# Optimization experiments

Hardware: AMD Instinct MI355X
Metric: run time of the kernel (lower is better)

Reference implementation:

```python
import jax, jax.numpy as jnp
import numpy as np

B, TM1, D, H = 1024, 255, 128, 128  # batch, n_timestep-1, input_size, hidden_size


def setup_inputs() -> dict:
    key = jax.random.key(0)
    ks = jax.random.split(key, 7)
    s = 0.05
    return {
        "input_data": jax.random.normal(ks[0], (B, TM1, D), jnp.float32),
        "Wa": jax.random.normal(ks[1], (1, 2 * H + TM1), jnp.float32) * s,
        "ba": jax.random.normal(ks[2], (1,), jnp.float32) * s,
        "W_ih": jax.random.normal(ks[3], (4 * H, D), jnp.float32) * s,
        "W_hh": jax.random.normal(ks[4], (4 * H, H), jnp.float32) * s,
        "b_ih": jax.random.normal(ks[5], (4 * H,), jnp.float32) * s,
        "b_hh": jax.random.normal(ks[6], (4 * H,), jnp.float32) * s,
    }


def _encoder(input_data, Wa, ba, W_ih, W_hh, b_ih, b_hh):
    b, tm1, d = input_data.shape
    h_dim = W_hh.shape[1]
    # Split attention weight into hidden / cell / time-series parts.
    Wh, Wc, Wx = Wa[0, :h_dim], Wa[0, h_dim:2 * h_dim], Wa[0, 2 * h_dim:]
    # Contribution of the (constant across steps) full driving series: (B, D)
    x_part = jnp.einsum("btd,t->bd", input_data, Wx)

    def step(carry, x_t):  # x_t: (B, D) = input_data[:, t, :]
        h, c = carry  # each (B, H)
        # attn score[b, d] = Wh.h[b] + Wc.c[b] + Wx.x[b, :, d] + ba  -> (B, D)
        score = x_part + (h @ Wh)[:, None] + (c @ Wc)[:, None] + ba[0]
        attn = jax.nn.softmax(score, axis=1)
        wx = attn * x_t  # weighted input (B, D)
        # single LSTM cell step, PyTorch gate order i, f, g, o
        gates = wx @ W_ih.T + b_ih + h @ W_hh.T + b_hh  # (B, 4H)
        i, f, g, o = jnp.split(gates, 4, axis=1)
        c_new = jax.nn.sigmoid(f) * c + jax.nn.sigmoid(i) * jnp.tanh(g)
        h_new = jax.nn.sigmoid(o) * jnp.tanh(c_new)
        return (h_new, c_new), (wx, h_new)

    h0 = jnp.zeros((b, h_dim), input_data.dtype)
    c0 = jnp.zeros((b, h_dim), input_data.dtype)
    xs = jnp.transpose(input_data, (1, 0, 2))  # (T-1, B, D)
    _, (wts, enc) = jax.lax.scan(step, (h0, c0), xs)
    input_weighted = jnp.transpose(wts, (1, 0, 2))  # (B, T-1, D)
    input_encoded = jnp.transpose(enc, (1, 0, 2))   # (B, T-1, H)
    return input_weighted, input_encoded


def reference(input_data, Wa, ba, W_ih, W_hh, b_ih, b_hh):
    return _encoder(input_data, Wa, ba, W_ih, W_hh, b_ih, b_hh)
```

## Files before the change

kernel.cpp:

```cpp
#include <hip/hip_runtime.h>
#include <hip/hip_bf16.h>
#include <stdint.h>

#define B_ 1024
#define T_ 255
#define D_ 128

typedef float f32x4 __attribute__((ext_vector_type(4)));
typedef short s16x8 __attribute__((ext_vector_type(8)));
typedef unsigned u32x4 __attribute__((ext_vector_type(4)));

__device__ __forceinline__ unsigned pk2(float a, float b){
  __hip_bfloat162 h2 = __float22bfloat162_rn(make_float2(a, b));
  union { __hip_bfloat162 h; unsigned u; } c; c.h = h2; return c.u;
}
__device__ __forceinline__ unsigned short bf1(float a){
  __hip_bfloat16 h = __float2bfloat16(a);
  union { __hip_bfloat16 h; unsigned short u; } c; c.h = h; return c.u;
}
__device__ __forceinline__ float sigm_f(float x){
  return __builtin_amdgcn_rcpf(1.f + __expf(-x));
}
__device__ __forceinline__ float tanh_f2(float x){
  return fmaf(-2.f, __builtin_amdgcn_rcpf(1.f + __expf(2.f * x)), 1.f);
}

__global__ __launch_bounds__(512) void k_attn(const float* __restrict__ x,
    const float* __restrict__ Wa, float* __restrict__ out_w,
    uint2* __restrict__ wxq){
  extern __shared__ float4 xs4[];
  __shared__ float wxs[256];
  __shared__ float part_s[16][128];
  __shared__ float red[128];
  __shared__ float attn_s[128];
  int tid = threadIdx.x, b = blockIdx.x;
  if (tid < T_) wxs[tid] = Wa[2 * D_ + tid];
  __syncthreads();
  const float4* xg = (const float4*)(x + (size_t)b * T_ * D_);
  float4 acc = {0.f, 0.f, 0.f, 0.f};
  for (int i = tid; i < 8160; i += 512){
    float4 v = xg[i];
    xs4[i] = v;
    float wt = wxs[i >> 5];
    acc.x += v.x * wt; acc.y += v.y * wt; acc.z += v.z * wt; acc.w += v.w * wt;
  }
  int d0 = (tid & 31) * 4, s = tid >> 5;
  *(float4*)&part_s[s][d0] = acc;
  __syncthreads();
  if (tid < 128){
    float v = 0.f;
    #pragma unroll
    for (int k = 0; k < 16; k++) v += part_s[k][tid];
    red[tid] = v; attn_s[tid] = v;
  }
  __syncthreads();
  for (int st = 64; st >= 1; st >>= 1){
    if (tid < st) red[tid] = fmaxf(red[tid], red[tid + st]);
    __syncthreads();
  }
  float mx = red[0];
  __syncthreads();
  float ev = 0.f;
  if (tid < 128){ ev = __expf(attn_s[tid] - mx); red[tid] = ev; }
  __syncthreads();
  for (int st = 64; st >= 1; st >>= 1){
    if (tid < st) red[tid] += red[tid + st];
    __syncthreads();
  }
  float sm = red[0];
  if (tid < 128) attn_s[tid] = ev / sm;
  __syncthreads();
  float4 at = *(const float4*)&attn_s[d0];
  float4* owg = (float4*)(out_w + (size_t)b * T_ * D_);
  for (int i = tid; i < 8160; i += 512){
    float4 v = xs4[i];
    float4 wv; wv.x = v.x*at.x; wv.y = v.y*at.y; wv.z = v.z*at.z; wv.w = v.w*at.w;
    owg[i] = wv;
    int t = i >> 5;
    uint2 q;
    q.x = pk2(wv.x, wv.y);
    q.y = pk2(wv.z, wv.w);
    wxq[((size_t)t * B_ + b) * 32 + (i & 31)] = q;
  }
}

__global__ __launch_bounds__(512, 2) void k_rnn(const float* __restrict__ W_ih,
    const float* __restrict__ W_hh, const float* __restrict__ b_ih,
    const float* __restrict__ b_hh, const unsigned short* __restrict__ wxb,
    float* __restrict__ out_e){
  __shared__ char hl[2048];
  __shared__ float4 g1l[2048];
  int tid = threadIdx.x;
  int lane = tid & 63, w = tid >> 6;
  int l15 = lane & 15, lg = lane >> 4;
  int row0 = blockIdx.x << 2;
  int d = w * 16 + l15;
  int hr = l15 >> 2;

  s16x8 fih[4][4], fhh[4][4];
  float bias[4];
  #pragma unroll
  for (int g = 0; g < 4; g++){
    int n = g * 128 + w * 16 + l15;
    bias[g] = b_ih[n] + b_hh[n];
    #pragma unroll
    for (int kt = 0; kt < 4; kt++){
      const float4* p1 = (const float4*)(W_ih + n * D_ + kt * 32 + lg * 8);
      float4 a0 = p1[0], a1 = p1[1];
      u32x4 bv;
      bv[0] = pk2(a0.x, a0.y); bv[1] = pk2(a0.z, a0.w);
      bv[2] = pk2(a1.x, a1.y); bv[3] = pk2(a1.z, a1.w);
      fih[kt][g] = __builtin_bit_cast(s16x8, bv);
      const float4* p2 = (const float4*)(W_hh + n * D_ + kt * 32 + lg * 8);
      float4 c0v = p2[0], c1v = p2[1];
      u32x4 cv;
      cv[0] = pk2(c0v.x, c0v.y); cv[1] = pk2(c0v.z, c0v.w);
      cv[2] = pk2(c1v.x, c1v.y); cv[3] = pk2(c1v.z, c1v.w);
      fhh[kt][g] = __builtin_bit_cast(s16x8, cv);
    }
  }
  unsigned rd_[4];
  #pragma unroll
  for (int kt = 0; kt < 4; kt++)
    rd_[kt] = (unsigned)(hr * 256 + (((kt << 2) + lg) ^ ((hr & 1) << 2)) * 16);
  unsigned wr_ = (unsigned)(lg * 256 + ((d >> 3) ^ ((lg & 1) << 2)) * 16 + (d & 7) * 2);

  float* op = out_e + (size_t)(row0 + lg) * T_ * D_ + d;
  float cst = 0.f;
  if (tid < 128) ((uint2*)hl)[tid] = make_uint2(0u, 0u);

  int gw0 = lg * 512 + d;
  int gr0 = lg * 128 + d;

  const unsigned short* wpb = wxb + ((size_t)(l15 >> 2) * B_ + row0 + (l15 & 3)) * D_ + lg * 8;
  const size_t GSTRIDE = (size_t)4 * B_ * D_;
  s16x8 AF0[4], AF1[4];
  #pragma unroll
  for (int kt = 0; kt < 4; kt++) AF0[kt] = *(const s16x8*)(wpb + kt * 32);
  #pragma unroll
  for (int kt = 0; kt < 4; kt++) AF1[kt] = *(const s16x8*)(wpb + GSTRIDE + kt * 32);
  __syncthreads();

#define BAR() do {                                                                  \
    asm volatile("s_waitcnt lgkmcnt(0)" ::: "memory");                              \
    __builtin_amdgcn_s_barrier();                                                   \
  } while (0)

#define FIH_BATCH(AF) do {                                                          \
    f32x4 bi = {bias[0], bias[0], bias[0], bias[0]};                                \
    f32x4 bf = {bias[1], bias[1], bias[1], bias[1]};                                \
    f32x4 bg = {bias[2], bias[2], bias[2], bias[2]};                                \
    f32x4 bo = {bias[3], bias[3], bias[3], bias[3]};                                \
    _Pragma("unroll")                                                               \
    for (int kt = 0; kt < 4; kt++){                                                 \
      bi = __builtin_amdgcn_mfma_f32_16x16x32_bf16(AF[kt], fih[kt][0], bi,0,0,0);   \
      bf = __builtin_amdgcn_mfma_f32_16x16x32_bf16(AF[kt], fih[kt][1], bf,0,0,0);   \
      bg = __builtin_amdgcn_mfma_f32_16x16x32_bf16(AF[kt], fih[kt][2], bg,0,0,0);   \
      bo = __builtin_amdgcn_mfma_f32_16x16x32_bf16(AF[kt], fih[kt][3], bo,0,0,0);   \
    }                                                                               \
    _Pragma("unroll")                                                               \
    for (int r = 0; r < 4; r++)                                                     \
      g1l[gw0 + r * 128] = make_float4(bi[r], bf[r], bg[r], bo[r]);                 \
  } while (0)

#define STEP(TS) do {                                                               \
    s16x8 aa[4];                                                                    \
    _Pragma("unroll")                                                               \
    for (int kt = 0; kt < 4; kt++)                                                  \
      aa[kt] = *(const s16x8*)(hl + rd_[kt] + ((TS) & 1) * 1024);                   \
    f32x4 a0 = {0.f,0.f,0.f,0.f}, a1 = a0, a2 = a0, a3 = a0;                        \
    _Pragma("unroll")                                                               \
    for (int kt = 0; kt < 4; kt++){                                                 \
      a0 = __builtin_amdgcn_mfma_f32_16x16x32_bf16(aa[kt], fhh[kt][0], a0,0,0,0);   \
      a1 = __builtin_amdgcn_mfma_f32_16x16x32_bf16(aa[kt], fhh[kt][1], a1,0,0,0);   \
      a2 = __builtin_amdgcn_mfma_f32_16x16x32_bf16(aa[kt], fhh[kt][2], a2,0,0,0);   \
      a3 = __builtin_amdgcn_mfma_f32_16x16x32_bf16(aa[kt], fhh[kt][3], a3,0,0,0);   \
    }                                                                               \
    float4 q = g1l[gr0 + (TS) * 512];                                               \
    float gi = q.x + a0[0], gf = q.y + a1[0];                                       \
    float gg = q.z + a2[0], go = q.w + a3[0];                                       \
    float cn = fmaf(sigm_f(gf), cst, sigm_f(gi) * tanh_f2(gg));                     \
    float hn = sigm_f(go) * tanh_f2(cn); cst = cn;                                  \
    *op = hn; op += D_;                                                             \
    *(unsigned short*)(hl + wr_ + (1 - ((TS) & 1)) * 1024) = bf1(hn);               \
    BAR();                                                                          \
  } while (0)

  for (int g = 0; g < 62; g += 2){
    FIH_BATCH(AF0);
    #pragma unroll
    for (int kt = 0; kt < 4; kt++)
      AF0[kt] = *(const s16x8*)(wpb + (size_t)(g + 2) * GSTRIDE + kt * 32);
    STEP(0); STEP(1); STEP(2); STEP(3);
    FIH_BATCH(AF1);
    #pragma unroll
    for (int kt = 0; kt < 4; kt++)
      AF1[kt] = *(const s16x8*)(wpb + (size_t)(g + 3) * GSTRIDE + kt * 32);
    STEP(0); STEP(1); STEP(2); STEP(3);
  }
  FIH_BATCH(AF0);
  STEP(0); STEP(1); STEP(2); STEP(3);
  FIH_BATCH(AF1);
  STEP(0); STEP(1); STEP(2);
#undef FIH_BATCH
#undef STEP
#undef BAR
}

extern "C" void kernel_launch(void* const* d_in, const int* in_sizes, int n_in,
                              void* d_out, int out_size, void* d_ws, size_t ws_size,
                              hipStream_t stream) {
  (void)in_sizes; (void)n_in; (void)out_size;
  const float* x    = (const float*)d_in[0];
  const float* Wa   = (const float*)d_in[1];
  const float* W_ih = (const float*)d_in[3];
  const float* W_hh = (const float*)d_in[4];
  const float* b_ih = (const float*)d_in[5];
  const float* b_hh = (const float*)d_in[6];
  float* out_w = (float*)d_out;
  float* out_e = out_w + (size_t)B_ * T_ * D_;
  unsigned short* wxb = (unsigned short*)d_ws;
  size_t need = (size_t)(T_ + 1) * B_ * D_ * 2;
  if (ws_size < need) return;

  hipMemsetAsync((char*)d_ws + (size_t)T_ * B_ * D_ * 2, 0, (size_t)B_ * D_ * 2, stream);
  k_attn<<<B_, 512, 130560, stream>>>(x, Wa, out_w, (uint2*)wxb);
  k_rnn <<<256, 512, 0, stream>>>(W_ih, W_hh, b_ih, b_hh, wxb, out_e);
}
```

Baseline: 237.5 us.

## Halve RNN block to four waves, each computing 32 hidden columns

The recurrent kernel now launches 256 threads per block instead of 512. Each wave owns two 16-column slices of the hidden state, so it holds twice as many bf16 weight fragments in registers and issues twice as many MFMAs per step. It also runs the LSTM cell update for two columns. The aim is to make the per-step barrier cheaper by having fewer waves synchronise. The cost is a longer serial MFMA and elementwise chain per wave on the latency-bound recurrence, plus much higher register pressure.

```diff
diff --git a/kernel.cpp b/kernel.cpp
--- a/kernel.cpp
+++ b/kernel.cpp
@@ -84,7 +84,7 @@
   }
 }
 
-__global__ __launch_bounds__(512, 2) void k_rnn(const float* __restrict__ W_ih,
+__global__ __launch_bounds__(256, 1) void k_rnn(const float* __restrict__ W_ih,
     const float* __restrict__ W_hh, const float* __restrict__ b_ih,
     const float* __restrict__ b_hh, const unsigned short* __restrict__ wxb,
     float* __restrict__ out_e){
@@ -94,43 +94,47 @@
   int lane = tid & 63, w = tid >> 6;
   int l15 = lane & 15, lg = lane >> 4;
   int row0 = blockIdx.x << 2;
-  int d = w * 16 + l15;
+  int d0 = w * 32 + l15, d1 = d0 + 16;
   int hr = l15 >> 2;
 
-  s16x8 fih[4][4], fhh[4][4];
-  float bias[4];
+  s16x8 fih[4][4][2], fhh[4][4][2];
+  float bias[4][2];
   #pragma unroll
   for (int g = 0; g < 4; g++){
-    int n = g * 128 + w * 16 + l15;
-    bias[g] = b_ih[n] + b_hh[n];
-    #pragma unroll
-    for (int kt = 0; kt < 4; kt++){
-      const float4* p1 = (const float4*)(W_ih + n * D_ + kt * 32 + lg * 8);
-      float4 a0 = p1[0], a1 = p1[1];
-      u32x4 bv;
-      bv[0] = pk2(a0.x, a0.y); bv[1] = pk2(a0.z, a0.w);
-      bv[2] = pk2(a1.x, a1.y); bv[3] = pk2(a1.z, a1.w);
-      fih[kt][g] = __builtin_bit_cast(s16x8, bv);
-      const float4* p2 = (const float4*)(W_hh + n * D_ + kt * 32 + lg * 8);
-      float4 c0v = p2[0], c1v = p2[1];
-      u32x4 cv;
-      cv[0] = pk2(c0v.x, c0v.y); cv[1] = pk2(c0v.z, c0v.w);
-      cv[2] = pk2(c1v.x, c1v.y); cv[3] = pk2(c1v.z, c1v.w);
-      fhh[kt][g] = __builtin_bit_cast(s16x8, cv);
+    #pragma unroll
+    for (int j = 0; j < 2; j++){
+      int n = g * 128 + w * 32 + j * 16 + l15;
+      bias[g][j] = b_ih[n] + b_hh[n];
+      #pragma unroll
+      for (int kt = 0; kt < 4; kt++){
+        const float4* p1 = (const float4*)(W_ih + n * D_ + kt * 32 + lg * 8);
+        float4 a0 = p1[0], a1 = p1[1];
+        u32x4 bv;
+        bv[0] = pk2(a0.x, a0.y); bv[1] = pk2(a0.z, a0.w);
+        bv[2] = pk2(a1.x, a1.y); bv[3] = pk2(a1.z, a1.w);
+        fih[kt][g][j] = __builtin_bit_cast(s16x8, bv);
+        const float4* p2 = (const float4*)(W_hh + n * D_ + kt * 32 + lg * 8);
+        float4 c0v = p2[0], c1v = p2[1];
+        u32x4 cv;
+        cv[0] = pk2(c0v.x, c0v.y); cv[1] = pk2(c0v.z, c0v.w);
+        cv[2] = pk2(c1v.x, c1v.y); cv[3] = pk2(c1v.z, c1v.w);
+        fhh[kt][g][j] = __builtin_bit_cast(s16x8, cv);
+      }
     }
   }
   unsigned rd_[4];
   #pragma unroll
   for (int kt = 0; kt < 4; kt++)
     rd_[kt] = (unsigned)(hr * 256 + (((kt << 2) + lg) ^ ((hr & 1) << 2)) * 16);
-  unsigned wr_ = (unsigned)(lg * 256 + ((d >> 3) ^ ((lg & 1) << 2)) * 16 + (d & 7) * 2);
-
-  float* op = out_e + (size_t)(row0 + lg) * T_ * D_ + d;
-  float cst = 0.f;
+  unsigned wr0 = (unsigned)(lg * 256 + ((d0 >> 3) ^ ((lg & 1) << 2)) * 16 + (d0 & 7) * 2);
+  unsigned wr1 = (unsigned)(lg * 256 + ((d1 >> 3) ^ ((lg & 1) << 2)) * 16 + (d1 & 7) * 2);
+
+  float* op = out_e + (size_t)(row0 + lg) * T_ * D_ + d0;
+  float c0s = 0.f, c1s = 0.f;
   if (tid < 128) ((uint2*)hl)[tid] = make_uint2(0u, 0u);
 
-  int gw0 = lg * 512 + d;
-  int gr0 = lg * 128 + d;
+  int gw0 = (lg * 4) * 128 + d0;
+  int gr0 = lg * 128 + d0;
 
   const unsigned short* wpb = wxb + ((size_t)(l15 >> 2) * B_ + row0 + (l15 & 3)) * D_ + lg * 8;
   const size_t GSTRIDE = (size_t)4 * B_ * D_;
@@ -147,20 +151,28 @@
   } while (0)
 
 #define FIH_BATCH(AF) do {                                                          \
-    f32x4 bi = {bias[0], bias[0], bias[0], bias[0]};                                \
-    f32x4 bf = {bias[1], bias[1], bias[1], bias[1]};                                \
-    f32x4 bg = {bias[2], bias[2], bias[2], bias[2]};                                \
-    f32x4 bo = {bias[3], bias[3], bias[3], bias[3]};                                \
-    _Pragma("unroll")                                                               \
-    for (int kt = 0; kt < 4; kt++){                                                 \
-      bi = __builtin_amdgcn_mfma_f32_16x16x32_bf16(AF[kt], fih[kt][0], bi,0,0,0);   \
-      bf = __builtin_amdgcn_mfma_f32_16x16x32_bf16(AF[kt], fih[kt][1], bf,0,0,0);   \
-      bg = __builtin_amdgcn_mfma_f32_16x16x32_bf16(AF[kt], fih[kt][2], bg,0,0,0);   \
-      bo = __builtin_amdgcn_mfma_f32_16x16x32_bf16(AF[kt], fih[kt][3], bo,0,0,0);   \
-    }                                                                               \
+    f32x4 bacc[4][2];                                                               \
+    _Pragma("unroll")                                                               \
+    for (int g = 0; g < 4; g++)                                                     \
+      _Pragma("unroll")                                                             \
+      for (int j = 0; j < 2; j++){                                                  \
+        float bb = bias[g][j];                                                      \
+        bacc[g][j] = (f32x4){bb, bb, bb, bb};                                       \
+      }                                                                             \
+    _Pragma("unroll")                                                               \
+    for (int kt = 0; kt < 4; kt++)                                                  \
+      _Pragma("unroll")                                                             \
+      for (int g = 0; g < 4; g++)                                                   \
+        _Pragma("unroll")                                                           \
+        for (int j = 0; j < 2; j++)                                                 \
+          bacc[g][j] = __builtin_amdgcn_mfma_f32_16x16x32_bf16(                     \
+                         AF[kt], fih[kt][g][j], bacc[g][j], 0, 0, 0);               \
     _Pragma("unroll")                                                               \
     for (int r = 0; r < 4; r++)                                                     \
-      g1l[gw0 + r * 128] = make_float4(bi[r], bf[r], bg[r], bo[r]);                 \
+      _Pragma("unroll")                                                             \
+      for (int j = 0; j < 2; j++)                                                   \
+        g1l[gw0 + r * 128 + j * 16] = make_float4(                                  \
+            bacc[0][j][r], bacc[1][j][r], bacc[2][j][r], bacc[3][j][r]);            \
   } while (0)
 
 #define STEP(TS) do {                                                               \
@@ -168,21 +180,34 @@
     _Pragma("unroll")                                                               \
     for (int kt = 0; kt < 4; kt++)                                                  \
       aa[kt] = *(const s16x8*)(hl + rd_[kt] + ((TS) & 1) * 1024);                   \
-    f32x4 a0 = {0.f,0.f,0.f,0.f}, a1 = a0, a2 = a0, a3 = a0;                        \
-    _Pragma("unroll")                                                               \
-    for (int kt = 0; kt < 4; kt++){                                                 \
-      a0 = __builtin_amdgcn_mfma_f32_16x16x32_bf16(aa[kt], fhh[kt][0], a0,0,0,0);   \
-      a1 = __builtin_amdgcn_mfma_f32_16x16x32_bf16(aa[kt], fhh[kt][1], a1,0,0,0);   \
-      a2 = __builtin_amdgcn_mfma_f32_16x16x32_bf16(aa[kt], fhh[kt][2], a2,0,0,0);   \
-      a3 = __builtin_amdgcn_mfma_f32_16x16x32_bf16(aa[kt], fhh[kt][3], a3,0,0,0);   \
-    }                                                                               \
-    float4 q = g1l[gr0 + (TS) * 512];                                               \
-    float gi = q.x + a0[0], gf = q.y + a1[0];                                       \
-    float gg = q.z + a2[0], go = q.w + a3[0];                                       \
-    float cn = fmaf(sigm_f(gf), cst, sigm_f(gi) * tanh_f2(gg));                     \
-    float hn = sigm_f(go) * tanh_f2(cn); cst = cn;                                  \
-    *op = hn; op += D_;                                                             \
-    *(unsigned short*)(hl + wr_ + (1 - ((TS) & 1)) * 1024) = bf1(hn);               \
+    f32x4 acc[4][2];                                                                \
+    _Pragma("unroll")                                                               \
+    for (int g = 0; g < 4; g++)                                                     \
+      _Pragma("unroll")                                                             \
+      for (int j = 0; j < 2; j++) acc[g][j] = (f32x4){0.f, 0.f, 0.f, 0.f};          \
+    _Pragma("unroll")                                                               \
+    for (int kt = 0; kt < 4; kt++)                                                  \
+      _Pragma("unroll")                                                             \
+      for (int g = 0; g < 4; g++)                                                   \
+        _Pragma("unroll")                                                           \
+        for (int j = 0; j < 2; j++)                                                 \
+          acc[g][j] = __builtin_amdgcn_mfma_f32_16x16x32_bf16(                      \
+                        aa[kt], fhh[kt][g][j], acc[g][j], 0, 0, 0);                 \
+    float4 q0 = g1l[gr0 + (TS) * 512];                                              \
+    float4 q1 = g1l[gr0 + (TS) * 512 + 16];                                         \
+    { float gi = q0.x + acc[0][0][0], gf = q0.y + acc[1][0][0];                     \
+      float gg = q0.z + acc[2][0][0], go = q0.w + acc[3][0][0];                     \
+      float cn = fmaf(sigm_f(gf), c0s, sigm_f(gi) * tanh_f2(gg));                   \
+      float hn = sigm_f(go) * tanh_f2(cn); c0s = cn;                                \
+      op[0] = hn;                                                                   \
+      *(unsigned short*)(hl + wr0 + (1 - ((TS) & 1)) * 1024) = bf1(hn); }           \
+    { float gi = q1.x + acc[0][1][0], gf = q1.y + acc[1][1][0];                     \
+      float gg = q1.z + acc[2][1][0], go = q1.w + acc[3][1][0];                     \
+      float cn = fmaf(sigm_f(gf), c1s, sigm_f(gi) * tanh_f2(gg));                   \
+      float hn = sigm_f(go) * tanh_f2(cn); c1s = cn;                                \
+      op[16] = hn;                                                                  \
+      *(unsigned short*)(hl + wr1 + (1 - ((TS) & 1)) * 1024) = bf1(hn); }           \
+    op += D_;                                                                       \
     BAR();                                                                          \
   } while (0)
 
@@ -225,5 +250,5 @@
 
   hipMemsetAsync((char*)d_ws + (size_t)T_ * B_ * D_ * 2, 0, (size_t)B_ * D_ * 2, stream);
   k_attn<<<B_, 512, 130560, stream>>>(x, Wa, out_w, (uint2*)wxb);
-  k_rnn <<<256, 512, 0, stream>>>(W_ih, W_hh, b_ih, b_hh, wxb, out_e);
-}
+  k_rnn <<<256, 256, 0, stream>>>(W_ih, W_hh, b_ih, b_hh, wxb, out_e);
+}
```

After: 310.2 us. 1.31x slower.
